# Kernel optimization log

Hardware: AMD Instinct MI355X
Metric: run time of the kernel (lower is better)

Reference implementation:

```python
import jax, jax.numpy as jnp
import numpy as np

# Module constants from init_kwargs
TAU = 10.0
THR = 1.0
WIDTH_GRAD = 1.0   # beta of SingleExponential surrogate
SCALE_GRAD = 1.0   # grad_scale of SingleExponential surrogate
ALPHA = float(np.exp(-1.0 / TAU))  # leak factor used by both ExpLeak and LIF


@jax.custom_vjp
def spike(v):
    # sinabs SingleSpike: at most one spike per timestep
    return (v >= THR).astype(v.dtype)

def _spike_fwd(v):
    return spike(v), v

def _spike_bwd(v, g):
    # SingleExponential surrogate gradient
    return (g * SCALE_GRAD * jnp.exp(-WIDTH_GRAD * jnp.abs(v - THR)),)

spike.defvjp(_spike_fwd, _spike_bwd)


def setup_inputs() -> dict:
    key = jax.random.key(0)
    k1, k2 = jax.random.split(key)
    x = jax.random.normal(k1, (32768, 2, 4, 4, 100), dtype=jnp.float32)
    w = jax.random.normal(k2, (1, 32), dtype=jnp.float32)
    return {"x": x, "w": w}


def reference(x, w):
    # x: (B, 2, 4, 4, T); w: (1, 32) -- slayer dense = per-timestep linear 32 -> 1
    B, T = x.shape[0], x.shape[-1]
    xf = x.reshape(B, -1, T)                      # (B, 32, T)
    weighted = jnp.einsum('bft,of->bot', xf, w)   # (B, 1, T)
    i_seq = jnp.moveaxis(weighted, -1, 0)         # (T, B, 1) time-major for scan
    v0 = jnp.zeros_like(i_seq[0])

    # ExpLeak: v[t] = alpha * v[t-1] + i[t]
    def leak_step(v, i_t):
        v = ALPHA * v + i_t
        return v, v

    _, syn = jax.lax.scan(leak_step, v0, i_seq)   # (T, B, 1) synaptic currents

    # LIF (norm_input=True): v[t] = alpha*v[t-1] + (1-alpha)*i[t];
    # SingleSpike threshold crossing, MembraneSubtract reset.
    def lif_step(v, i_t):
        v = ALPHA * v + (1.0 - ALPHA) * i_t
        s = spike(v)
        return v - THR * s, s

    _, spikes = jax.lax.scan(lif_step, v0, syn)   # (T, B, 1)
    return jnp.moveaxis(spikes, 0, -1)            # (B, 1, T)
```

## Files before the change

kernel.cpp:

```cpp
#include <hip/hip_runtime.h>


constexpr int T_STEPS = 100;
constexpr int F_IN    = 32;
constexpr int NB      = 64;
constexpr int BLOCK   = 256;
constexpr int QT      = T_STEPS / 4;
constexpr int ROWF    = T_STEPS + 4;

__global__ __launch_bounds__(BLOCK) void snn_fused(
    const float* __restrict__ x,
    const float* __restrict__ w,
    float* __restrict__ out)
{
#pragma clang fp contract(off)
    __shared__ float sw[NB * ROWF];

    const int tid = threadIdx.x;
    const long long b0 = (long long)blockIdx.x * NB;

    float wf[F_IN];
#pragma unroll
    for (int f = 0; f < F_IN; ++f) wf[f] = w[f];

    for (int i = tid; i < NB * QT; i += BLOCK) {
        const int nb = i / QT;
        const int j  = i - nb * QT;
        const float* xb = x + (b0 + nb) * (long long)(F_IN * T_STEPS) + 4 * j;
        float a0 = 0.0f, a1 = 0.0f, a2 = 0.0f, a3 = 0.0f;
#pragma unroll
        for (int f = 0; f < F_IN; ++f) {
            const float4 xv = *(const float4*)(xb + f * T_STEPS);
            a0 = a0 + xv.x * wf[f];
            a1 = a1 + xv.y * wf[f];
            a2 = a2 + xv.z * wf[f];
            a3 = a3 + xv.w * wf[f];
        }
        float4* dst = (float4*)(sw + nb * ROWF + 4 * j);
        *dst = make_float4(a0, a1, a2, a3);
    }
    __syncthreads();

    if (tid < NB) {
        const double ALPHA64 = 0.90483741803595957316;
        const float  A   = (float)ALPHA64;
        const float  OMA = (float)(1.0 - ALPHA64);
        float syn = 0.0f, v = 0.0f;
        const float* row = sw + tid * ROWF;
        float4* op = (float4*)(out + (b0 + tid) * (long long)T_STEPS);
#pragma unroll
        for (int q = 0; q < QT; ++q) {
            float4 s4;
            float* sp = (float*)&s4;
#pragma unroll
            for (int k = 0; k < 4; ++k) {
                syn = (A * syn) + row[4 * q + k];
                v   = (A * v) + (OMA * syn);
                const float s = (v >= 1.0f) ? 1.0f : 0.0f;
                v = v - s;
                sp[k] = s;
            }
            op[q] = s4;
        }
    }
}

extern "C" void kernel_launch(void* const* d_in, const int* in_sizes, int n_in,
                              void* d_out, int out_size, void* d_ws, size_t ws_size,
                              hipStream_t stream) {
    const float* x  = (const float*)d_in[0];
    const float* w  = (const float*)d_in[1];
    float* out      = (float*)d_out;
    const int B       = in_sizes[0] / (F_IN * T_STEPS);
    const int nblocks = B / NB;
    snn_fused<<<nblocks, BLOCK, 0, stream>>>(x, w, out);
}
```

Measured before the change: 544.9 us.

## Stage small per-block input slab through LDS with coalesced nontemporal loads

```diff
diff --git a/kernel.cpp b/kernel.cpp
--- a/kernel.cpp
+++ b/kernel.cpp
@@ -1,12 +1,16 @@
 #include <hip/hip_runtime.h>
 
 
+typedef float vf4 __attribute__((ext_vector_type(4)));
+
 constexpr int T_STEPS = 100;
 constexpr int F_IN    = 32;
-constexpr int NB      = 64;
-constexpr int BLOCK   = 256;
+constexpr int NB      = 4;
+constexpr int BLOCK   = 128;
 constexpr int QT      = T_STEPS / 4;
 constexpr int ROWF    = T_STEPS + 4;
+constexpr int SLABF   = NB * F_IN * T_STEPS;
+constexpr int CHUNKS  = SLABF / (4 * BLOCK);
 
 __global__ __launch_bounds__(BLOCK) void snn_fused(
     const float* __restrict__ x,
@@ -14,30 +18,42 @@
     float* __restrict__ out)
 {
 #pragma clang fp contract(off)
-    __shared__ float sw[NB * ROWF];
+    __shared__ float xs[SLABF];
+    __shared__ float cur[NB * ROWF];
 
     const int tid = threadIdx.x;
-    const long long b0 = (long long)blockIdx.x * NB;
+    const long long blk = blockIdx.x;
+    const float* slab = x + blk * (long long)SLABF;
+
+    vf4 v[CHUNKS];
+#pragma unroll
+    for (int c = 0; c < CHUNKS; ++c)
+        v[c] = __builtin_nontemporal_load((const vf4*)slab + c * BLOCK + tid);
+#pragma unroll
+    for (int c = 0; c < CHUNKS; ++c)
+        ((vf4*)xs)[c * BLOCK + tid] = v[c];
 
     float wf[F_IN];
 #pragma unroll
     for (int f = 0; f < F_IN; ++f) wf[f] = w[f];
 
-    for (int i = tid; i < NB * QT; i += BLOCK) {
-        const int nb = i / QT;
-        const int j  = i - nb * QT;
-        const float* xb = x + (b0 + nb) * (long long)(F_IN * T_STEPS) + 4 * j;
+    __syncthreads();
+
+    if (tid < NB * QT) {
+        const int nb = tid / QT;
+        const int j  = tid - nb * QT;
+        const float* xr = xs + nb * (F_IN * T_STEPS) + 4 * j;
         float a0 = 0.0f, a1 = 0.0f, a2 = 0.0f, a3 = 0.0f;
 #pragma unroll
         for (int f = 0; f < F_IN; ++f) {
-            const float4 xv = *(const float4*)(xb + f * T_STEPS);
+            const vf4 xv = *(const vf4*)(xr + f * T_STEPS);
             a0 = a0 + xv.x * wf[f];
             a1 = a1 + xv.y * wf[f];
             a2 = a2 + xv.z * wf[f];
             a3 = a3 + xv.w * wf[f];
         }
-        float4* dst = (float4*)(sw + nb * ROWF + 4 * j);
-        *dst = make_float4(a0, a1, a2, a3);
+        vf4* dst = (vf4*)(cur + nb * ROWF + 4 * j);
+        *dst = vf4{a0, a1, a2, a3};
     }
     __syncthreads();
 
@@ -45,20 +61,19 @@
         const double ALPHA64 = 0.90483741803595957316;
         const float  A   = (float)ALPHA64;
         const float  OMA = (float)(1.0 - ALPHA64);
-        float syn = 0.0f, v = 0.0f;
-        const float* row = sw + tid * ROWF;
-        float4* op = (float4*)(out + (b0 + tid) * (long long)T_STEPS);
+        float syn = 0.0f, vmem = 0.0f;
+        const float* row = cur + tid * ROWF;
+        vf4* op = (vf4*)(out + (blk * NB + tid) * (long long)T_STEPS);
 #pragma unroll
         for (int q = 0; q < QT; ++q) {
-            float4 s4;
-            float* sp = (float*)&s4;
+            vf4 s4;
 #pragma unroll
             for (int k = 0; k < 4; ++k) {
-                syn = (A * syn) + row[4 * q + k];
-                v   = (A * v) + (OMA * syn);
-                const float s = (v >= 1.0f) ? 1.0f : 0.0f;
-                v = v - s;
-                sp[k] = s;
+                syn  = (A * syn) + row[4 * q + k];
+                vmem = (A * vmem) + (OMA * syn);
+                const float s = (vmem >= 1.0f) ? 1.0f : 0.0f;
+                vmem = vmem - s;
+                s4[k] = s;
             }
             op[q] = s4;
         }
```

Measured after the change: 519.1 us. 1.05x faster.
